# Kernel optimization log

Hardware: AMD Instinct MI355X
Metric: run time of the kernel (lower is better)

Reference implementation:

```python
import jax, jax.numpy as jnp
import numpy as np

MD = 4          # search_range -> (2*MD+1)^2 = 81 correlation channels
DISP = 192      # disp_range   -> 192 horizontal displacement channels
NEG_SLOPE = 0.1


def bilinear_warp(x, flow):
    """Warp x [B,C,H,W] by pixel-offset flow [B,2,H,W] (x-offset=ch0, y-offset=ch1),
    bilinear, zeros outside (matches tf.grid_sample padding_mode='zeros')."""
    B, C, H, W = x.shape
    yy, xx = jnp.meshgrid(jnp.arange(H, dtype=x.dtype), jnp.arange(W, dtype=x.dtype), indexing='ij')
    gx = xx[None] + flow[:, 0]  # [B,H,W]
    gy = yy[None] + flow[:, 1]
    x0 = jnp.floor(gx); y0 = jnp.floor(gy)
    wx = gx - x0; wy = gy - y0
    x0i = x0.astype(jnp.int32); y0i = y0.astype(jnp.int32)

    def gather(img, xi, yi):  # img [C,H,W], xi/yi [H,W]
        valid = (xi >= 0) & (xi < W) & (yi >= 0) & (yi < H)
        xc = jnp.clip(xi, 0, W - 1); yc = jnp.clip(yi, 0, H - 1)
        return img[:, yc, xc] * valid[None].astype(img.dtype)

    def warp_one(img, x0i, y0i, wx, wy):
        v00 = gather(img, x0i,     y0i)
        v01 = gather(img, x0i + 1, y0i)
        v10 = gather(img, x0i,     y0i + 1)
        v11 = gather(img, x0i + 1, y0i + 1)
        return (v00 * (1 - wx) * (1 - wy) + v01 * wx * (1 - wy)
                + v10 * (1 - wx) * wy + v11 * wx * wy)

    return jax.vmap(warp_one)(x, x0i, y0i, wx, wy)


def corr_volume(a, b, md=MD):
    """FlowNet-style cost volume: sum over channels of a * shifted(b), zero-padded.
    a,b: [B,C,H,W] -> [B,(2md+1)^2,H,W]."""
    B, C, H, W = a.shape
    bp = jnp.pad(b, ((0, 0), (0, 0), (md, md), (md, md)))
    offs = jnp.stack(jnp.meshgrid(jnp.arange(2 * md + 1), jnp.arange(2 * md + 1),
                                  indexing='ij'), -1).reshape(-1, 2)

    def one(off):
        shifted = jax.lax.dynamic_slice(bp, (0, 0, off[0], off[1]), (B, C, H, W))
        return jnp.sum(a * shifted, axis=1)  # [B,H,W]

    return jnp.transpose(jax.vmap(one)(offs), (1, 0, 2, 3))


def disp_corr_volume(a, b, disp=DISP):
    """SpatialCorrelationSampler patch_size=(1,disp): horizontal-only cost volume,
    offsets dx in [-disp//2, disp//2 - 1]. -> [B,disp,H,W]."""
    B, C, H, W = a.shape
    half = disp // 2
    bp = jnp.pad(b, ((0, 0), (0, 0), (0, 0), (half, disp - 1 - half)))

    def one(dx):
        shifted = jax.lax.dynamic_slice(bp, (0, 0, 0, dx), (B, C, H, W))
        return jnp.sum(a * shifted, axis=1)

    return jnp.transpose(jax.vmap(one)(jnp.arange(disp)), (1, 0, 2, 3))


def lrelu(x):
    return jnp.where(x >= 0, x, NEG_SLOPE * x)


def setup_inputs() -> dict:
    key = jax.random.key(0)
    k1, k2, k3, k4 = jax.random.split(key, 4)
    B, C, H, W = 4, 64, 128, 416
    return {
        'x1': jax.random.normal(k1, (B, C, H, W), jnp.float32),
        'x2': jax.random.normal(k2, (B, C, H, W), jnp.float32),
        'r1': jax.random.normal(k3, (B, C, H, W), jnp.float32),
        'flow': jax.random.normal(k4, (B, 2, H, W), jnp.float32) * 2.0,
    }


def reference(x1, x2, r1, flow):
    x2_warp = bilinear_warp(x2, flow)                 # warping-layer grid sample
    out_corr_f = lrelu(corr_volume(x1, x2_warp))      # [B,81,H,W]
    disp_corr1 = lrelu(disp_corr_volume(x1, r1))      # [B,192,H,W]
    return jnp.concatenate([out_corr_f, disp_corr1], axis=1)  # [B,273,H,W]
```

## Files before the change

### kernel.cpp

```cpp
#include <hip/hip_runtime.h>

#define Wd 416
#define Hd 128
#define Cd 64
#define HWd 53248

typedef __attribute__((ext_vector_type(8))) short short8;
typedef __attribute__((ext_vector_type(4))) float f32x4;

union frag8 { short8 s; unsigned int u[4]; };

__device__ __forceinline__ float bf2f(unsigned short u) {
    unsigned int v = ((unsigned int)u) << 16;
    return __builtin_bit_cast(float, v);
}
__device__ __forceinline__ unsigned short f2bf(float f) {
    unsigned int u = __builtin_bit_cast(unsigned int, f);
    u += 0x7fffu + ((u >> 16) & 1u);
    return (unsigned short)(u >> 16);
}
__device__ __forceinline__ unsigned int pk2(float lo, float hi) {
    return (unsigned int)f2bf(lo) | ((unsigned int)f2bf(hi) << 16);
}
__device__ __forceinline__ float lrelu(float v) { return (v >= 0.f) ? v : 0.1f * v; }

__device__ __forceinline__ void wave_fence() {
    asm volatile("s_waitcnt lgkmcnt(0)" ::: "memory");
    __builtin_amdgcn_sched_barrier(0);
}

__global__ __launch_bounds__(256) void warp_k(const float* __restrict__ x2,
                                              const float* __restrict__ flow,
                                              unsigned short* __restrict__ x2wT) {
    int gid = blockIdx.x * 256 + threadIdx.x;
    int j = gid & 7;
    int p = gid >> 3;
    int x = p % Wd;
    int t = p / Wd;
    int y = t & 127;
    int b = t >> 7;

    int fbase = ((b * 2) * Hd + y) * Wd + x;
    float fx = flow[fbase];
    float fy = flow[fbase + HWd];
    float gx = (float)x + fx;
    float gy = (float)y + fy;
    float fx0 = floorf(gx), fy0 = floorf(gy);
    float wx = gx - fx0, wy = gy - fy0;
    int x0 = (int)fx0, y0 = (int)fy0;
    bool vx0 = (unsigned)x0 < (unsigned)Wd, vx1 = (unsigned)(x0 + 1) < (unsigned)Wd;
    bool vy0 = (unsigned)y0 < (unsigned)Hd, vy1 = (unsigned)(y0 + 1) < (unsigned)Hd;
    int cx0 = min(max(x0, 0), Wd - 1), cx1 = min(max(x0 + 1, 0), Wd - 1);
    int cy0 = min(max(y0, 0), Hd - 1), cy1 = min(max(y0 + 1, 0), Hd - 1);
    float w00 = (1.f - wx) * (1.f - wy) * ((vx0 && vy0) ? 1.f : 0.f);
    float w01 = wx * (1.f - wy) * ((vx1 && vy0) ? 1.f : 0.f);
    float w10 = (1.f - wx) * wy * ((vx0 && vy1) ? 1.f : 0.f);
    float w11 = wx * wy * ((vx1 && vy1) ? 1.f : 0.f);
    int o00 = cy0 * Wd + cx0, o01 = cy0 * Wd + cx1;
    int o10 = cy1 * Wd + cx0, o11 = cy1 * Wd + cx1;

    const float* base = x2 + (long)(b * Cd + j * 8) * HWd;
    unsigned int res[4];
#pragma unroll
    for (int cc = 0; cc < 8; cc++) {
        const float* pc = base + cc * HWd;
        float v = w00 * pc[o00] + w01 * pc[o01] + w10 * pc[o10] + w11 * pc[o11];
        unsigned short h = f2bf(v);
        if (cc & 1) res[cc >> 1] |= ((unsigned int)h) << 16;
        else        res[cc >> 1] = h;
    }
    *(uint4*)(x2wT + ((long)p * Cd + j * 8)) = make_uint4(res[0], res[1], res[2], res[3]);
}

__global__ __launch_bounds__(512, 4) void disp_k(const float* __restrict__ x1,
                                                 const float* __restrict__ r1,
                                                 float* __restrict__ out) {
    __shared__ unsigned short Bs[Wd * 64];
    __shared__ unsigned short Ds[8][96 * 16];

    int tid = threadIdx.x;
    int lane = tid & 63;
    int wv = tid >> 6;
    int m = lane & 15;
    int q = lane >> 4;

    int bid = blockIdx.x;
    int b = bid >> 7;
    int y = bid & 127;

    const float* Arow = x1 + ((long)(b * Cd) * Hd + y) * Wd;
    const float* Brow = r1 + ((long)(b * Cd) * Hd + y) * Wd;

    for (int idx = tid; idx < 8 * Wd; idx += 512) {
        int x = idx % Wd;
        int oc = idx / Wd;
        const float* pb = Brow + (long)(oc * 8) * HWd + x;
        unsigned int wb[4];
#pragma unroll
        for (int e = 0; e < 4; e++)
            wb[e] = pk2(pb[(2 * e) * HWd], pb[(2 * e + 1) * HWd]);
        *(uint4*)&Bs[x * 64 + ((oc ^ (x & 7)) * 8)] = make_uint4(wb[0], wb[1], wb[2], wb[3]);
    }

    frag8 a0[4], a1[4];
#pragma unroll
    for (int t = 0; t < 4; t++) {
        int i = wv + 8 * t;
        if (i < 26) {
            const float* pa = Arow + 16 * i + m;
#pragma unroll
            for (int k = 0; k < 4; k++) {
                a0[t].u[k] = pk2(pa[(8 * q + 2 * k) * HWd], pa[(8 * q + 2 * k + 1) * HWd]);
                a1[t].u[k] = pk2(pa[(32 + 8 * q + 2 * k) * HWd], pa[(32 + 8 * q + 2 * k + 1) * HWd]);
            }
        }
    }
    __syncthreads();

    unsigned short* Dw = Ds[wv];
#pragma unroll
    for (int h = 0; h < 2; h++) {
#pragma unroll
        for (int t = 0; t < 4; t++) {
            int i = wv + 8 * t;
            if (i >= 26) continue;
#pragma unroll
            for (int z = 0; z < 3; z++)
                *(uint4*)&Dw[(lane + 64 * z) * 8] = make_uint4(0, 0, 0, 0);
            wave_fence();
#pragma unroll
            for (int gg = 0; gg < 7; gg++) {
                int g = h ? gg : gg - 6;
                int jj = i + g;
                if ((unsigned)jj >= 26u) continue;
                int xp = 16 * jj + m;
                const unsigned short* bp = &Bs[xp * 64];
                short8 b0 = *(const short8*)(bp + ((q ^ (xp & 7)) * 8));
                short8 b1 = *(const short8*)(bp + (((q + 4) ^ (xp & 7)) * 8));
                f32x4 acc = {0.f, 0.f, 0.f, 0.f};
                acc = __builtin_amdgcn_mfma_f32_16x16x32_bf16(a0[t].s, b0, acc, 0, 0, 0);
                acc = __builtin_amdgcn_mfma_f32_16x16x32_bf16(a1[t].s, b1, acc, 0, 0, 0);
                int dbase = 16 * g + m - 4 * q + 96 - 96 * h;
#pragma unroll
                for (int r = 0; r < 4; r++) {
                    int d = dbase - r;
                    if ((unsigned)d < 96u)
                        Dw[d * 16 + 4 * q + r] = f2bf(lrelu(acc[r]));
                }
            }
            wave_fence();
            long chb = ((long)(b * 273 + 81 + 96 * h) * Hd + y) * Wd + 16 * i;
#pragma unroll
            for (int k = 0; k < 12; k++) {
                int e = 64 * k + lane;
                unsigned int w = *(unsigned int*)&Dw[e * 2];
                int d = e >> 3, xx = (e & 7) * 2;
                *(float2*)(out + chb + (long)d * HWd + xx) =
                    make_float2(bf2f((unsigned short)(w & 0xffffu)),
                                bf2f((unsigned short)(w >> 16)));
            }
            wave_fence();
        }
    }
}

__global__ __launch_bounds__(512, 4) void corr_k(const float* __restrict__ x1,
                                                 const unsigned short* __restrict__ x2wT,
                                                 float* __restrict__ out) {
    __shared__ unsigned short Bs[2][224 * 64];
    __shared__ unsigned short Cs[8][160];

    int tid = threadIdx.x;
    int lane = tid & 63;
    int wv = tid >> 6;
    int m = lane & 15;
    int q = lane >> 4;

    int bid = blockIdx.x;
    int b = bid & 3;
    int y2 = (bid >> 2) & 63;
    int xh = bid >> 8;
    int y0 = y2 * 2;
    int xbase = xh * 208;

    int yy = wv & 1;
    int it0 = wv >> 1;

    frag8 a0[4], a1[4];
#pragma unroll
    for (int t = 0; t < 4; t++) {
        int it = it0 + 4 * t;
        if (it < 13) {
            const float* pa = x1 + ((long)(b * Cd) * Hd + (y0 + yy)) * Wd + xbase + 16 * it + m;
#pragma unroll
            for (int k = 0; k < 4; k++) {
                a0[t].u[k] = pk2(pa[(8 * q + 2 * k) * HWd], pa[(8 * q + 2 * k + 1) * HWd]);
                a1[t].u[k] = pk2(pa[(32 + 8 * q + 2 * k) * HWd], pa[(32 + 8 * q + 2 * k + 1) * HWd]);
            }
        }
    }

    auto stage = [&](int yp, int sel) {
        int yg = y0 - 4 + yp;
        bool yok = (unsigned)yg < (unsigned)Hd;
        for (int idx = tid; idx < 224 * 8; idx += 512) {
            int pl = idx >> 3, oc = idx & 7;
            int xg = xbase - 4 + pl;
            uint4 v = make_uint4(0, 0, 0, 0);
            if (yok && (unsigned)xg < (unsigned)Wd)
                v = *(const uint4*)(x2wT + (((long)(b * Hd + yg) * Wd + xg) * Cd + oc * 8));
            *(uint4*)&Bs[sel][pl * 64 + ((oc ^ (pl & 7)) * 8)] = v;
        }
    };

    stage(0, 0);
    __syncthreads();

    for (int yp = 0; yp < 10; yp++) {
        int cur = yp & 1;
        if (yp < 9) stage(yp + 1, cur ^ 1);
        int dy = yp - 4 - yy;
        if ((unsigned)(dy + 4) <= 8u) {
            long obase = ((long)(b * 273 + (dy + 4) * 9) * Hd + (y0 + yy)) * Wd + xbase;
#pragma unroll
            for (int t = 0; t < 4; t++) {
                int it = it0 + 4 * t;
                if (it >= 13) continue;
#pragma unroll
                for (int dj = 0; dj < 2; dj++) {
                    int pl = 16 * (it + dj) + m;
                    const unsigned short* bp = &Bs[cur][pl * 64];
                    short8 b0 = *(const short8*)(bp + ((q ^ (pl & 7)) * 8));
                    short8 b1 = *(const short8*)(bp + (((q + 4) ^ (pl & 7)) * 8));
                    f32x4 acc = {0.f, 0.f, 0.f, 0.f};
                    acc = __builtin_amdgcn_mfma_f32_16x16x32_bf16(a0[t].s, b0, acc, 0, 0, 0);
                    acc = __builtin_amdgcn_mfma_f32_16x16x32_bf16(a1[t].s, b1, acc, 0, 0, 0);
                    int dbase = 16 * dj + m - 4 * q;
#pragma unroll
                    for (int r = 0; r < 4; r++) {
                        int dx4 = dbase - r;
                        if ((unsigned)dx4 <= 8u)
                            Cs[wv][dx4 * 16 + 4 * q + r] = f2bf(lrelu(acc[r]));
                    }
                }
                wave_fence();
#pragma unroll
                for (int k = 0; k < 2; k++) {
                    int e = 64 * k + lane;
                    if (e < 72) {
                        unsigned int w = *(unsigned int*)&Cs[wv][e * 2];
                        int dxr = e >> 3, xx = (e & 7) * 2;
                        *(float2*)(out + obase + (long)dxr * HWd + 16 * it + xx) =
                            make_float2(bf2f((unsigned short)(w & 0xffffu)),
                                        bf2f((unsigned short)(w >> 16)));
                    }
                }
                wave_fence();
            }
        }
        __syncthreads();
    }
}

extern "C" void kernel_launch(void* const* d_in, const int* in_sizes, int n_in,
                              void* d_out, int out_size, void* d_ws, size_t ws_size,
                              hipStream_t stream) {
    const float* x1 = (const float*)d_in[0];
    const float* x2 = (const float*)d_in[1];
    const float* r1 = (const float*)d_in[2];
    const float* fl = (const float*)d_in[3];
    float* out = (float*)d_out;
    unsigned short* x2wT = (unsigned short*)d_ws;

    warp_k<<<6656, 256, 0, stream>>>(x2, fl, x2wT);
    disp_k<<<512, 512, 0, stream>>>(x1, r1, out);
    corr_k<<<512, 512, 0, stream>>>(x1, x2wT, out);
}
```

Before: 480.0 us.

## Fuse disp and corr kernels into one interleaved launch; change warped layout

Merges the disparity and correlation kernels into a single launch whose blocks alternate between the two workloads, sharing a union of their shared-memory layouts, so the two phases overlap and one launch and its tail are removed. The warp kernel now writes the warped tensor as channel-group-major planes, with consecutive threads at consecutive x, which should coalesce its flow and gather reads better; the corr staging loads are re-indexed to match. The disp path also skips zero-filling its staging buffer for interior tiles where every entry is overwritten. The union makes every block reserve the larger disp footprint, which may reduce occupancy for corr blocks.

```diff
diff --git a/kernel.cpp b/kernel.cpp
--- a/kernel.cpp
+++ b/kernel.cpp
@@ -32,13 +32,13 @@
 __global__ __launch_bounds__(256) void warp_k(const float* __restrict__ x2,
                                               const float* __restrict__ flow,
                                               unsigned short* __restrict__ x2wT) {
-    int gid = blockIdx.x * 256 + threadIdx.x;
-    int j = gid & 7;
-    int p = gid >> 3;
-    int x = p % Wd;
-    int t = p / Wd;
-    int y = t & 127;
-    int b = t >> 7;
+    int idx = blockIdx.x * 256 + threadIdx.x;
+    int x = idx % Wd;
+    int r = idx / Wd;
+    int y = r & 127;
+    int s = r >> 7;
+    int oc = s & 7;
+    int b = s >> 3;
 
     int fbase = ((b * 2) * Hd + y) * Wd + x;
     float fx = flow[fbase];
@@ -59,7 +59,7 @@
     int o00 = cy0 * Wd + cx0, o01 = cy0 * Wd + cx1;
     int o10 = cy1 * Wd + cx0, o11 = cy1 * Wd + cx1;
 
-    const float* base = x2 + (long)(b * Cd + j * 8) * HWd;
+    const float* base = x2 + (long)(b * Cd + oc * 8) * HWd;
     unsigned int res[4];
 #pragma unroll
     for (int cc = 0; cc < 8; cc++) {
@@ -69,22 +69,29 @@
         if (cc & 1) res[cc >> 1] |= ((unsigned int)h) << 16;
         else        res[cc >> 1] = h;
     }
-    *(uint4*)(x2wT + ((long)p * Cd + j * 8)) = make_uint4(res[0], res[1], res[2], res[3]);
-}
-
-__global__ __launch_bounds__(512, 4) void disp_k(const float* __restrict__ x1,
-                                                 const float* __restrict__ r1,
-                                                 float* __restrict__ out) {
-    __shared__ unsigned short Bs[Wd * 64];
-    __shared__ unsigned short Ds[8][96 * 16];
-
+    *(uint4*)(x2wT + ((long)idx * 8)) = make_uint4(res[0], res[1], res[2], res[3]);
+}
+
+struct DispSmem {
+    unsigned short Bs[Wd * 64];
+    unsigned short Ds[8][96 * 16];
+};
+struct CorrSmem {
+    unsigned short Bs[2][224 * 64];
+    unsigned short Cs[8][160];
+};
+union FusedSmem { DispSmem d; CorrSmem c; };
+
+__device__ __forceinline__ void disp_body(int bid, DispSmem& S,
+                                          const float* __restrict__ x1,
+                                          const float* __restrict__ r1,
+                                          float* __restrict__ out) {
     int tid = threadIdx.x;
     int lane = tid & 63;
     int wv = tid >> 6;
     int m = lane & 15;
     int q = lane >> 4;
 
-    int bid = blockIdx.x;
     int b = bid >> 7;
     int y = bid & 127;
 
@@ -99,7 +106,7 @@
 #pragma unroll
         for (int e = 0; e < 4; e++)
             wb[e] = pk2(pb[(2 * e) * HWd], pb[(2 * e + 1) * HWd]);
-        *(uint4*)&Bs[x * 64 + ((oc ^ (x & 7)) * 8)] = make_uint4(wb[0], wb[1], wb[2], wb[3]);
+        *(uint4*)&S.Bs[x * 64 + ((oc ^ (x & 7)) * 8)] = make_uint4(wb[0], wb[1], wb[2], wb[3]);
     }
 
     frag8 a0[4], a1[4];
@@ -117,24 +124,27 @@
     }
     __syncthreads();
 
-    unsigned short* Dw = Ds[wv];
+    unsigned short* Dw = S.Ds[wv];
 #pragma unroll
     for (int h = 0; h < 2; h++) {
 #pragma unroll
         for (int t = 0; t < 4; t++) {
             int i = wv + 8 * t;
             if (i >= 26) continue;
-#pragma unroll
-            for (int z = 0; z < 3; z++)
-                *(uint4*)&Dw[(lane + 64 * z) * 8] = make_uint4(0, 0, 0, 0);
-            wave_fence();
+            bool interior = h ? (i <= 19) : (i >= 6);
+            if (!interior) {
+#pragma unroll
+                for (int z = 0; z < 3; z++)
+                    *(uint4*)&Dw[(lane + 64 * z) * 8] = make_uint4(0, 0, 0, 0);
+                wave_fence();
+            }
 #pragma unroll
             for (int gg = 0; gg < 7; gg++) {
                 int g = h ? gg : gg - 6;
                 int jj = i + g;
                 if ((unsigned)jj >= 26u) continue;
                 int xp = 16 * jj + m;
-                const unsigned short* bp = &Bs[xp * 64];
+                const unsigned short* bp = &S.Bs[xp * 64];
                 short8 b0 = *(const short8*)(bp + ((q ^ (xp & 7)) * 8));
                 short8 b1 = *(const short8*)(bp + (((q + 4) ^ (xp & 7)) * 8));
                 f32x4 acc = {0.f, 0.f, 0.f, 0.f};
@@ -164,19 +174,16 @@
     }
 }
 
-__global__ __launch_bounds__(512, 4) void corr_k(const float* __restrict__ x1,
-                                                 const unsigned short* __restrict__ x2wT,
-                                                 float* __restrict__ out) {
-    __shared__ unsigned short Bs[2][224 * 64];
-    __shared__ unsigned short Cs[8][160];
-
+__device__ __forceinline__ void corr_body(int bid, CorrSmem& S,
+                                          const float* __restrict__ x1,
+                                          const unsigned short* __restrict__ x2wT,
+                                          float* __restrict__ out) {
     int tid = threadIdx.x;
     int lane = tid & 63;
     int wv = tid >> 6;
     int m = lane & 15;
     int q = lane >> 4;
 
-    int bid = blockIdx.x;
     int b = bid & 3;
     int y2 = (bid >> 2) & 63;
     int xh = bid >> 8;
@@ -203,13 +210,13 @@
     auto stage = [&](int yp, int sel) {
         int yg = y0 - 4 + yp;
         bool yok = (unsigned)yg < (unsigned)Hd;
-        for (int idx = tid; idx < 224 * 8; idx += 512) {
-            int pl = idx >> 3, oc = idx & 7;
+        for (int idx = tid; idx < 8 * 224; idx += 512) {
+            int oc = idx / 224, pl = idx - oc * 224;
             int xg = xbase - 4 + pl;
             uint4 v = make_uint4(0, 0, 0, 0);
             if (yok && (unsigned)xg < (unsigned)Wd)
-                v = *(const uint4*)(x2wT + (((long)(b * Hd + yg) * Wd + xg) * Cd + oc * 8));
-            *(uint4*)&Bs[sel][pl * 64 + ((oc ^ (pl & 7)) * 8)] = v;
+                v = *(const uint4*)(x2wT + ((((long)(b * 8 + oc) * Hd + yg) * Wd + xg) * 8));
+            *(uint4*)&S.Bs[sel][pl * 64 + ((oc ^ (pl & 7)) * 8)] = v;
         }
     };
 
@@ -229,7 +236,7 @@
 #pragma unroll
                 for (int dj = 0; dj < 2; dj++) {
                     int pl = 16 * (it + dj) + m;
-                    const unsigned short* bp = &Bs[cur][pl * 64];
+                    const unsigned short* bp = &S.Bs[cur][pl * 64];
                     short8 b0 = *(const short8*)(bp + ((q ^ (pl & 7)) * 8));
                     short8 b1 = *(const short8*)(bp + (((q + 4) ^ (pl & 7)) * 8));
                     f32x4 acc = {0.f, 0.f, 0.f, 0.f};
@@ -240,7 +247,7 @@
                     for (int r = 0; r < 4; r++) {
                         int dx4 = dbase - r;
                         if ((unsigned)dx4 <= 8u)
-                            Cs[wv][dx4 * 16 + 4 * q + r] = f2bf(lrelu(acc[r]));
+                            S.Cs[wv][dx4 * 16 + 4 * q + r] = f2bf(lrelu(acc[r]));
                     }
                 }
                 wave_fence();
@@ -248,7 +255,7 @@
                 for (int k = 0; k < 2; k++) {
                     int e = 64 * k + lane;
                     if (e < 72) {
-                        unsigned int w = *(unsigned int*)&Cs[wv][e * 2];
+                        unsigned int w = *(unsigned int*)&S.Cs[wv][e * 2];
                         int dxr = e >> 3, xx = (e & 7) * 2;
                         *(float2*)(out + obase + (long)dxr * HWd + 16 * it + xx) =
                             make_float2(bf2f((unsigned short)(w & 0xffffu)),
@@ -260,6 +267,16 @@
         }
         __syncthreads();
     }
+}
+
+__global__ __launch_bounds__(512, 4) void fused_k(const float* __restrict__ x1,
+                                                  const float* __restrict__ r1,
+                                                  const unsigned short* __restrict__ x2wT,
+                                                  float* __restrict__ out) {
+    __shared__ FusedSmem sm;
+    int bid = blockIdx.x;
+    if ((bid & 1) == 0) disp_body(bid >> 1, sm.d, x1, r1, out);
+    else                corr_body(bid >> 1, sm.c, x1, x2wT, out);
 }
 
 extern "C" void kernel_launch(void* const* d_in, const int* in_sizes, int n_in,
@@ -273,6 +290,5 @@
     unsigned short* x2wT = (unsigned short*)d_ws;
 
     warp_k<<<6656, 256, 0, stream>>>(x2, fl, x2wT);
-    disp_k<<<512, 512, 0, stream>>>(x1, r1, out);
-    corr_k<<<512, 512, 0, stream>>>(x1, x2wT, out);
-}
+    fused_k<<<1024, 512, 0, stream>>>(x1, r1, x2wT, out);
+}
```

Measured after the change: 456.8 us. 4.8% less time.
